# Kernel tuning notes

Measured on AMD Instinct MI355X. Metric: run time of the kernel, lower is better.

## Reference

```python
import jax, jax.numpy as jnp
import numpy as np

NEG_INF = jnp.float32(-(2.0**32) + 1.0)


def squash(z):
    # z: [B, k_max, out_units]
    sq_norm = jnp.sum(jnp.square(z), axis=-1, keepdims=True)
    scale = sq_norm / (1.0 + sq_norm) / jnp.sqrt(sq_norm + 1e-8)
    return scale * z


def setup_inputs() -> dict:
    key = jax.random.key(0)
    k1, k2, k3, k4 = jax.random.split(key, 4)
    B, L, D_IN, D_OUT, K = 1024, 200, 256, 256, 8
    behavior_embeddings = jax.random.normal(k1, (B, L, D_IN), dtype=jnp.float32)
    seq_len = jax.random.randint(k2, (B, 1), 1, L + 1, dtype=jnp.int32)
    routing_logits = jax.random.normal(k3, (1, K, L), dtype=jnp.float32)  # init_std=1.0
    bilinear_mapping_matrix = jax.random.normal(k4, (D_IN, D_OUT), dtype=jnp.float32)
    return {
        "behavior_embeddings": behavior_embeddings,
        "seq_len": seq_len,
        "routing_logits": routing_logits,
        "bilinear_mapping_matrix": bilinear_mapping_matrix,
    }


def reference(behavior_embeddings, seq_len, routing_logits, bilinear_mapping_matrix):
    ITERATION_TIMES = 3
    B, L, _ = behavior_embeddings.shape
    K = routing_logits.shape[1]

    # mask: [B, 1, L] broadcastable to [B, K, L] (same seq_len for every capsule)
    mask = jnp.arange(L)[None, None, :] < seq_len[:, :, None]

    # bilinear map is loop-invariant: [B, L, out_units]
    mapped = jnp.einsum("ble,eo->blo", behavior_embeddings, bilinear_mapping_matrix)

    logits = routing_logits  # [1, K, L]
    interest_capsules = None
    for _ in range(ITERATION_TIMES):
        logits_pad = jnp.where(mask, jnp.broadcast_to(logits, (B, K, L)), NEG_INF)
        weight = jax.nn.softmax(logits_pad, axis=-1)          # [B, K, L]
        Z = jnp.einsum("bkl,blo->bko", weight, mapped)         # [B, K, out]
        interest_capsules = squash(Z)                          # [B, K, out]
        # delta: sum over batch of capsules @ mapped^T -> [1, K, L]
        delta = jnp.einsum("bko,blo->kl", interest_capsules, mapped)[None]
        logits = logits + delta  # emulates assign_add on non-trainable B

    return interest_capsules.reshape(-1, K, interest_capsules.shape[-1])
```

## Files before the change

### kernel.cpp

```cpp
#include <hip/hip_runtime.h>
#include <cstdint>
#include <cstddef>

#define B_    1024
#define L_    200
#define DIN_  256
#define DOUT_ 256
#define K_    8
#define M_    (B_ * L_)

typedef __attribute__((ext_vector_type(8))) short bf16x8;
typedef __attribute__((ext_vector_type(4))) float f32x4;

__device__ __forceinline__ float bf2f(unsigned short u) {
  union { unsigned int i; float f; } w; w.i = ((unsigned int)u) << 16; return w.f;
}
__device__ __forceinline__ unsigned short f2bf(float f) {
  union { float f; unsigned int i; } w; w.f = f;
  unsigned int x = w.i;
  return (unsigned short)((x + 0x7fffu + ((x >> 16) & 1u)) >> 16);
}

__global__ __launch_bounds__(256)
void wt_prep(const float* __restrict__ W, unsigned short* __restrict__ Wh,
             unsigned short* __restrict__ Wm, unsigned short* __restrict__ Wl)
{
  const int k = blockIdx.x;
  const int n = threadIdx.x;
  float x = W[k * DOUT_ + n];
  unsigned short h = f2bf(x);
  float r = x - bf2f(h);
  unsigned short m = f2bf(r);
  float r2 = r - bf2f(m);
  unsigned short l = f2bf(r2);
  const int k0b = k >> 5, quad = (k >> 3) & 3, j = k & 7;
  const int nt = n >> 4, lr = n & 15;
  const size_t idx = ((((size_t)k0b * 16 + nt) * 64) + (quad * 16 + lr)) * 8 + j;
  Wh[idx] = h;
  Wm[idx] = m;
  Wl[idx] = l;
}

__global__ __launch_bounds__(256, 2)
void gemm_mapped(const float* __restrict__ A,
                 const unsigned short* __restrict__ Wh,
                 const unsigned short* __restrict__ Wm,
                 const unsigned short* __restrict__ Wl,
                 float* __restrict__ C)
{
  const int t    = threadIdx.x;
  const int wave = t >> 6;
  const int lane = t & 63;
  const int quad = lane >> 4;
  const int lr   = lane & 15;
  const int m0   = blockIdx.x * 128 + wave * 32;

  f32x4 acc[2][16];
  #pragma unroll
  for (int mt = 0; mt < 2; ++mt)
    #pragma unroll
    for (int nt = 0; nt < 16; ++nt)
      acc[mt][nt] = (f32x4){0.f, 0.f, 0.f, 0.f};

  bf16x8 Bh[4], Bm[4], Bl[4];
  bf16x8 ah[2], am[2], al[2];
  float4 Af[2][2];

#define BLOAD(K0B, NT, S) do { \
    const size_t _off = (((size_t)(K0B) * 16 + (NT)) * 64 + lane) * 8; \
    Bh[S] = *(const bf16x8*)(Wh + _off); \
    Bm[S] = *(const bf16x8*)(Wm + _off); \
    Bl[S] = *(const bf16x8*)(Wl + _off); \
  } while (0)

  const float* ap0 = A + (size_t)(m0 + lr) * DIN_ + quad * 8;
  const float* ap1 = A + (size_t)(m0 + 16 + lr) * DIN_ + quad * 8;

  Af[0][0] = *(const float4*)(ap0);
  Af[0][1] = *(const float4*)(ap0 + 4);
  Af[1][0] = *(const float4*)(ap1);
  Af[1][1] = *(const float4*)(ap1 + 4);
  BLOAD(0, 0, 0); BLOAD(0, 1, 1); BLOAD(0, 2, 2); BLOAD(0, 3, 3);

  for (int k0b = 0; k0b < 8; ++k0b) {
    #pragma unroll
    for (int mt = 0; mt < 2; ++mt) {
      float xs[8] = {Af[mt][0].x, Af[mt][0].y, Af[mt][0].z, Af[mt][0].w,
                     Af[mt][1].x, Af[mt][1].y, Af[mt][1].z, Af[mt][1].w};
      #pragma unroll
      for (int j = 0; j < 8; ++j) {
        unsigned short h = f2bf(xs[j]);
        float r = xs[j] - bf2f(h);
        unsigned short mm = f2bf(r);
        float r2 = r - bf2f(mm);
        unsigned short ll = f2bf(r2);
        ah[mt][j] = (short)h; am[mt][j] = (short)mm; al[mt][j] = (short)ll;
      }
    }
    if (k0b < 7) {
      const int ko = (k0b + 1) * 32;
      Af[0][0] = *(const float4*)(ap0 + ko);
      Af[0][1] = *(const float4*)(ap0 + ko + 4);
      Af[1][0] = *(const float4*)(ap1 + ko);
      Af[1][1] = *(const float4*)(ap1 + ko + 4);
    }

#define GROUP(NT, S) do { \
    f32x4 c0 = acc[0][NT], c1 = acc[1][NT]; \
    c0 = __builtin_amdgcn_mfma_f32_16x16x32_bf16(ah[0], Bh[S], c0, 0, 0, 0); \
    c1 = __builtin_amdgcn_mfma_f32_16x16x32_bf16(ah[1], Bh[S], c1, 0, 0, 0); \
    c0 = __builtin_amdgcn_mfma_f32_16x16x32_bf16(ah[0], Bm[S], c0, 0, 0, 0); \
    c1 = __builtin_amdgcn_mfma_f32_16x16x32_bf16(ah[1], Bm[S], c1, 0, 0, 0); \
    c0 = __builtin_amdgcn_mfma_f32_16x16x32_bf16(am[0], Bh[S], c0, 0, 0, 0); \
    c1 = __builtin_amdgcn_mfma_f32_16x16x32_bf16(am[1], Bh[S], c1, 0, 0, 0); \
    c0 = __builtin_amdgcn_mfma_f32_16x16x32_bf16(ah[0], Bl[S], c0, 0, 0, 0); \
    c1 = __builtin_amdgcn_mfma_f32_16x16x32_bf16(ah[1], Bl[S], c1, 0, 0, 0); \
    c0 = __builtin_amdgcn_mfma_f32_16x16x32_bf16(am[0], Bm[S], c0, 0, 0, 0); \
    c1 = __builtin_amdgcn_mfma_f32_16x16x32_bf16(am[1], Bm[S], c1, 0, 0, 0); \
    c0 = __builtin_amdgcn_mfma_f32_16x16x32_bf16(al[0], Bh[S], c0, 0, 0, 0); \
    c1 = __builtin_amdgcn_mfma_f32_16x16x32_bf16(al[1], Bh[S], c1, 0, 0, 0); \
    acc[0][NT] = c0; acc[1][NT] = c1; \
  } while (0)

    GROUP(0, 0);  BLOAD(k0b, 4, 0);
    GROUP(1, 1);  BLOAD(k0b, 5, 1);
    GROUP(2, 2);  BLOAD(k0b, 6, 2);
    GROUP(3, 3);  BLOAD(k0b, 7, 3);
    GROUP(4, 0);  BLOAD(k0b, 8, 0);
    GROUP(5, 1);  BLOAD(k0b, 9, 1);
    GROUP(6, 2);  BLOAD(k0b, 10, 2);
    GROUP(7, 3);  BLOAD(k0b, 11, 3);
    GROUP(8, 0);  BLOAD(k0b, 12, 0);
    GROUP(9, 1);  BLOAD(k0b, 13, 1);
    GROUP(10, 2); BLOAD(k0b, 14, 2);
    GROUP(11, 3); BLOAD(k0b, 15, 3);
    GROUP(12, 0);
    GROUP(13, 1);
    GROUP(14, 2);
    GROUP(15, 3);
    if (k0b < 7) {
      BLOAD(k0b + 1, 0, 0); BLOAD(k0b + 1, 1, 1);
      BLOAD(k0b + 1, 2, 2); BLOAD(k0b + 1, 3, 3);
    }
#undef GROUP
  }
#undef BLOAD

  #pragma unroll
  for (int mt = 0; mt < 2; ++mt)
    #pragma unroll
    for (int nt = 0; nt < 16; ++nt)
      #pragma unroll
      for (int r = 0; r < 4; ++r) {
        int row = m0 + mt * 16 + quad * 4 + r;
        C[(size_t)row * DOUT_ + nt * 16 + lr] = acc[mt][nt][r];
      }
}

__global__ __launch_bounds__(256)
void z_kernel(const float* __restrict__ mapped, const float* __restrict__ logits,
              const int* __restrict__ seq_len, float* __restrict__ caps)
{
  const int t    = threadIdx.x;
  const int lane = t & 63;
  const int wave = t >> 6;
  const int b    = blockIdx.x * 4 + wave;
  const int len  = seq_len[b];
  __shared__ float w[4][K_][204];

  #pragma unroll
  for (int k = 0; k < K_; ++k) {
    float v[4];
    float mx = -3.4028235e38f;
    #pragma unroll
    for (int i = 0; i < 4; ++i) {
      int l = lane + 64 * i;
      v[i] = (l < len) ? logits[k * L_ + l] : -3.4028235e38f;
      mx = fmaxf(mx, v[i]);
    }
    #pragma unroll
    for (int s = 1; s < 64; s <<= 1) mx = fmaxf(mx, __shfl_xor(mx, s, 64));
    float e[4]; float sum = 0.f;
    #pragma unroll
    for (int i = 0; i < 4; ++i) {
      int l = lane + 64 * i;
      e[i] = (l < len) ? __expf(v[i] - mx) : 0.f;
      sum += e[i];
    }
    #pragma unroll
    for (int s = 1; s < 64; s <<= 1) sum += __shfl_xor(sum, s, 64);
    float inv = 1.f / sum;
    #pragma unroll
    for (int i = 0; i < 4; ++i) {
      int l = lane + 64 * i;
      if (l < 204) w[wave][k][l] = e[i] * inv;
    }
  }

  f32x4 acc[K_];
  #pragma unroll
  for (int k = 0; k < K_; ++k) acc[k] = (f32x4){0.f, 0.f, 0.f, 0.f};
  const float* mp = mapped + (size_t)b * L_ * DOUT_ + lane * 4;
  const int lceil = (len + 3) & ~3;
  for (int l = 0; l < lceil; l += 4) {
    float4 m0 = *(const float4*)(mp + (size_t)(l + 0) * DOUT_);
    float4 m1 = *(const float4*)(mp + (size_t)(l + 1) * DOUT_);
    float4 m2 = *(const float4*)(mp + (size_t)(l + 2) * DOUT_);
    float4 m3 = *(const float4*)(mp + (size_t)(l + 3) * DOUT_);
    #pragma unroll
    for (int k = 0; k < K_; ++k) {
      float4 wv = *(const float4*)&w[wave][k][l];
      f32x4 c = acc[k];
      c.x += wv.x * m0.x + wv.y * m1.x + wv.z * m2.x + wv.w * m3.x;
      c.y += wv.x * m0.y + wv.y * m1.y + wv.z * m2.y + wv.w * m3.y;
      c.z += wv.x * m0.z + wv.y * m1.z + wv.z * m2.z + wv.w * m3.z;
      c.w += wv.x * m0.w + wv.y * m1.w + wv.z * m2.w + wv.w * m3.w;
      acc[k] = c;
    }
  }

  #pragma unroll
  for (int k = 0; k < K_; ++k) {
    float sq = acc[k].x * acc[k].x + acc[k].y * acc[k].y
             + acc[k].z * acc[k].z + acc[k].w * acc[k].w;
    #pragma unroll
    for (int s = 1; s < 64; s <<= 1) sq += __shfl_xor(sq, s, 64);
    float scale = sq / ((1.f + sq) * sqrtf(sq + 1e-8f));
    float4 o;
    o.x = scale * acc[k].x; o.y = scale * acc[k].y;
    o.z = scale * acc[k].z; o.w = scale * acc[k].w;
    *(float4*)&caps[((size_t)b * K_ + k) * DOUT_ + lane * 4] = o;
  }
}

__global__ __launch_bounds__(256)
void delta_kernel(const float* __restrict__ mapped, const float* __restrict__ caps,
                  float* __restrict__ partials)
{
  const int t    = threadIdx.x;
  const int lane = t & 63;
  const int wave = t >> 6;
  const int wid  = blockIdx.x * 4 + wave;
  const int lc   = wid % 25;
  const int bc   = wid / 25;
  const int l0   = lc * 8;
  const int o4   = lane * 4;

  const float* cb = caps   + (size_t)(bc * 16) * (K_ * DOUT_) + o4;
  const float* mb = mapped + ((size_t)(bc * 16) * L_ + l0) * DOUT_ + o4;

  float acc[K_][8];
  #pragma unroll
  for (int k = 0; k < K_; ++k)
    #pragma unroll
    for (int ll = 0; ll < 8; ++ll) acc[k][ll] = 0.f;

  float4 cA[K_], mA[8], cB[K_], mB[8];

#define LOADC(DST, BI) do { \
    const float* _p = cb + (size_t)(BI) * (K_ * DOUT_); \
    _Pragma("unroll") \
    for (int _k = 0; _k < K_; ++_k) DST[_k] = *(const float4*)(_p + _k * DOUT_); \
  } while (0)
#define LOADM(DST, BI) do { \
    const float* _p = mb + (size_t)(BI) * (L_ * DOUT_); \
    _Pragma("unroll") \
    for (int _l = 0; _l < 8; ++_l) DST[_l] = *(const float4*)(_p + _l * DOUT_); \
  } while (0)
#define COMPUTE(CC, MM) do { \
    _Pragma("unroll") \
    for (int _k = 0; _k < K_; ++_k) \
      _Pragma("unroll") \
      for (int _l = 0; _l < 8; ++_l) \
        acc[_k][_l] += CC[_k].x * MM[_l].x + CC[_k].y * MM[_l].y \
                     + CC[_k].z * MM[_l].z + CC[_k].w * MM[_l].w; \
  } while (0)

  LOADC(cA, 0); LOADM(mA, 0);
  for (int i = 0; i < 8; ++i) {
    LOADC(cB, 2 * i + 1); LOADM(mB, 2 * i + 1);
    COMPUTE(cA, mA);
    if (i < 7) { LOADC(cA, 2 * i + 2); LOADM(mA, 2 * i + 2); }
    COMPUTE(cB, mB);
  }
#undef LOADC
#undef LOADM
#undef COMPUTE

  float out = 0.f;
  #pragma unroll
  for (int k = 0; k < K_; ++k)
    #pragma unroll
    for (int ll = 0; ll < 8; ++ll) {
      float v = acc[k][ll];
      v += __shfl_xor(v, 1, 64);
      v += __shfl_xor(v, 2, 64);
      v += __shfl_xor(v, 4, 64);
      v += __shfl_xor(v, 8, 64);
      v += __shfl_xor(v, 16, 64);
      v += __shfl_xor(v, 32, 64);
      if (lane == k * 8 + ll) out = v;
    }
  partials[((size_t)bc * K_ + (lane >> 3)) * L_ + l0 + (lane & 7)] = out;
}

__global__ __launch_bounds__(256)
void init_logits(const float* __restrict__ rlog, float* __restrict__ logits)
{
  int i = blockIdx.x * 256 + threadIdx.x;
  if (i < K_ * L_) logits[i] = rlog[i];
}

__global__ __launch_bounds__(256)
void reduce_kernel(const float* __restrict__ partials, float* __restrict__ logits)
{
  int i = blockIdx.x * 256 + threadIdx.x;
  if (i < K_ * L_) {
    float s = 0.f;
    #pragma unroll 4
    for (int bc = 0; bc < 64; ++bc) s += partials[bc * (K_ * L_) + i];
    logits[i] += s;
  }
}

extern "C" void kernel_launch(void* const* d_in, const int* in_sizes, int n_in,
                              void* d_out, int out_size, void* d_ws, size_t ws_size,
                              hipStream_t stream)
{
  const float* behav = (const float*)d_in[0];
  const int*   slen  = (const int*)d_in[1];
  const float* rlog  = (const float*)d_in[2];
  const float* W     = (const float*)d_in[3];
  float* caps = (float*)d_out;

  char* ws = (char*)d_ws;
  float* logitsW  = (float*)ws;
  float* partials = (float*)(ws + 8192);
  unsigned short* Wh = (unsigned short*)(ws + 458752);
  unsigned short* Wm = (unsigned short*)(ws + 589824);
  unsigned short* Wl = (unsigned short*)(ws + 720896);
  float* mapped   = (float*)(ws + (1 << 20));

  init_logits<<<dim3(7), 256, 0, stream>>>(rlog, logitsW);
  wt_prep<<<dim3(256), 256, 0, stream>>>(W, Wh, Wm, Wl);
  gemm_mapped<<<dim3(1600), 256, 0, stream>>>(behav, Wh, Wm, Wl, mapped);
  for (int it = 0; it < 3; ++it) {
    z_kernel<<<dim3(B_ / 4), 256, 0, stream>>>(mapped, logitsW, slen, caps);
    if (it < 2) {
      delta_kernel<<<dim3(400), 256, 0, stream>>>(mapped, caps, partials);
      reduce_kernel<<<dim3(7), 256, 0, stream>>>(partials, logitsW);
    }
  }
}
```

Baseline: 637.5 us.

## Fuse routing z and delta into one kernel with fixed-point atomic accumulation

Merges the capsule computation and the delta reduction into one per-batch kernel. Logit updates are accumulated via int64 fixed-point atomics instead of a partials buffer plus reduce kernel, and the z phase is restructured to one block per batch with waves splitting the sequence. This removes the separate delta and reduce launches and the caps round trip, at the cost of many contended global atomics and per-row wave shuffle reductions.

```diff
diff --git a/kernel.cpp b/kernel.cpp
--- a/kernel.cpp
+++ b/kernel.cpp
@@ -157,26 +157,45 @@
       }
 }
 
-__global__ __launch_bounds__(256)
-void z_kernel(const float* __restrict__ mapped, const float* __restrict__ logits,
-              const int* __restrict__ seq_len, float* __restrict__ caps)
+#define DSCALE     67108864.0f
+#define DSCALE_INV 1.4901161193847656e-8f
+
+template<bool DO_DELTA>
+__global__ __launch_bounds__(256, 4)
+void zdelta_kernel(const float* __restrict__ mapped,
+                   const float* __restrict__ rlog,
+                   const long long* __restrict__ accA,
+                   const long long* __restrict__ accB,
+                   const int* __restrict__ seq_len,
+                   long long* __restrict__ accOut,
+                   float* __restrict__ caps)
 {
   const int t    = threadIdx.x;
   const int lane = t & 63;
   const int wave = t >> 6;
-  const int b    = blockIdx.x * 4 + wave;
+  const int b    = blockIdx.x;
   const int len  = seq_len[b];
-  __shared__ float w[4][K_][204];
-
-  #pragma unroll
-  for (int k = 0; k < K_; ++k) {
+
+  __shared__ float wsmT[200][8];
+  __shared__ float zred[2][8][256];
+  __shared__ float capsL[8][256];
+  __shared__ float sqred[4][8];
+
+  #pragma unroll
+  for (int kk = 0; kk < 2; ++kk) {
+    const int k = wave * 2 + kk;
     float v[4];
     float mx = -3.4028235e38f;
     #pragma unroll
     for (int i = 0; i < 4; ++i) {
       int l = lane + 64 * i;
-      v[i] = (l < len) ? logits[k * L_ + l] : -3.4028235e38f;
-      mx = fmaxf(mx, v[i]);
+      float lv = -3.4028235e38f;
+      if (l < len) {
+        long long a = accA[(k * L_ + l) * 8] + accB[(k * L_ + l) * 8];
+        lv = rlog[k * L_ + l] + (float)a * DSCALE_INV;
+      }
+      v[i] = lv;
+      mx = fmaxf(mx, lv);
     }
     #pragma unroll
     for (int s = 1; s < 64; s <<= 1) mx = fmaxf(mx, __shfl_xor(mx, s, 64));
@@ -193,134 +212,91 @@
     #pragma unroll
     for (int i = 0; i < 4; ++i) {
       int l = lane + 64 * i;
-      if (l < 204) w[wave][k][l] = e[i] * inv;
-    }
-  }
-
-  f32x4 acc[K_];
-  #pragma unroll
-  for (int k = 0; k < K_; ++k) acc[k] = (f32x4){0.f, 0.f, 0.f, 0.f};
-  const float* mp = mapped + (size_t)b * L_ * DOUT_ + lane * 4;
-  const int lceil = (len + 3) & ~3;
-  for (int l = 0; l < lceil; l += 4) {
-    float4 m0 = *(const float4*)(mp + (size_t)(l + 0) * DOUT_);
-    float4 m1 = *(const float4*)(mp + (size_t)(l + 1) * DOUT_);
-    float4 m2 = *(const float4*)(mp + (size_t)(l + 2) * DOUT_);
-    float4 m3 = *(const float4*)(mp + (size_t)(l + 3) * DOUT_);
+      if (l < L_) wsmT[l][k] = e[i] * inv;
+    }
+  }
+  __syncthreads();
+
+  f32x4 zacc[K_];
+  #pragma unroll
+  for (int k = 0; k < K_; ++k) zacc[k] = (f32x4){0.f, 0.f, 0.f, 0.f};
+
+  const float* mp = mapped + (size_t)b * (L_ * DOUT_) + lane * 4;
+  for (int l = wave; l < len; l += 4) {
+    f32x4 m = *(const f32x4*)(mp + (size_t)l * DOUT_);
+    float4 w0 = *(const float4*)&wsmT[l][0];
+    float4 w1 = *(const float4*)&wsmT[l][4];
+    zacc[0] += w0.x * m; zacc[1] += w0.y * m;
+    zacc[2] += w0.z * m; zacc[3] += w0.w * m;
+    zacc[4] += w1.x * m; zacc[5] += w1.y * m;
+    zacc[6] += w1.z * m; zacc[7] += w1.w * m;
+  }
+
+  if (wave >= 2) {
+    #pragma unroll
+    for (int k = 0; k < K_; ++k)
+      *(f32x4*)&zred[wave - 2][k][lane * 4] = zacc[k];
+  }
+  __syncthreads();
+  if (wave < 2) {
     #pragma unroll
     for (int k = 0; k < K_; ++k) {
-      float4 wv = *(const float4*)&w[wave][k][l];
-      f32x4 c = acc[k];
-      c.x += wv.x * m0.x + wv.y * m1.x + wv.z * m2.x + wv.w * m3.x;
-      c.y += wv.x * m0.y + wv.y * m1.y + wv.z * m2.y + wv.w * m3.y;
-      c.z += wv.x * m0.z + wv.y * m1.z + wv.z * m2.z + wv.w * m3.z;
-      c.w += wv.x * m0.w + wv.y * m1.w + wv.z * m2.w + wv.w * m3.w;
-      acc[k] = c;
-    }
-  }
+      f32x4 r = *(const f32x4*)&zred[wave][k][lane * 4];
+      r += zacc[k];
+      *(f32x4*)&zred[wave][k][lane * 4] = r;
+    }
+  }
+  __syncthreads();
+
+  float z[K_];
+  #pragma unroll
+  for (int k = 0; k < K_; ++k) z[k] = zred[0][k][t] + zred[1][k][t];
 
   #pragma unroll
   for (int k = 0; k < K_; ++k) {
-    float sq = acc[k].x * acc[k].x + acc[k].y * acc[k].y
-             + acc[k].z * acc[k].z + acc[k].w * acc[k].w;
-    #pragma unroll
-    for (int s = 1; s < 64; s <<= 1) sq += __shfl_xor(sq, s, 64);
+    float s2 = z[k] * z[k];
+    #pragma unroll
+    for (int s = 1; s < 64; s <<= 1) s2 += __shfl_xor(s2, s, 64);
+    if (lane == 0) sqred[wave][k] = s2;
+  }
+  __syncthreads();
+  #pragma unroll
+  for (int k = 0; k < K_; ++k) {
+    float sq = sqred[0][k] + sqred[1][k] + sqred[2][k] + sqred[3][k];
     float scale = sq / ((1.f + sq) * sqrtf(sq + 1e-8f));
-    float4 o;
-    o.x = scale * acc[k].x; o.y = scale * acc[k].y;
-    o.z = scale * acc[k].z; o.w = scale * acc[k].w;
-    *(float4*)&caps[((size_t)b * K_ + k) * DOUT_ + lane * 4] = o;
+    float cv = scale * z[k];
+    if (DO_DELTA) capsL[k][t] = cv;
+    else caps[((size_t)b * K_ + k) * DOUT_ + t] = cv;
+  }
+
+  if constexpr (DO_DELTA) {
+    __syncthreads();
+    f32x4 cr[K_];
+    #pragma unroll
+    for (int k = 0; k < K_; ++k) cr[k] = *(const f32x4*)&capsL[k][lane * 4];
+
+    for (int l = wave; l < L_; l += 4) {
+      f32x4 m = *(const f32x4*)(mp + (size_t)l * DOUT_);
+      #pragma unroll
+      for (int k = 0; k < K_; ++k) {
+        float p = cr[k].x * m.x + cr[k].y * m.y + cr[k].z * m.z + cr[k].w * m.w;
+        #pragma unroll
+        for (int s = 1; s < 64; s <<= 1) p += __shfl_xor(p, s, 64);
+        if (lane == 0) {
+          long long q = llrintf(p * DSCALE);
+          atomicAdd((unsigned long long*)&accOut[(k * L_ + l) * 8],
+                    (unsigned long long)q);
+        }
+      }
+    }
   }
 }
 
 __global__ __launch_bounds__(256)
-void delta_kernel(const float* __restrict__ mapped, const float* __restrict__ caps,
-                  float* __restrict__ partials)
-{
-  const int t    = threadIdx.x;
-  const int lane = t & 63;
-  const int wave = t >> 6;
-  const int wid  = blockIdx.x * 4 + wave;
-  const int lc   = wid % 25;
-  const int bc   = wid / 25;
-  const int l0   = lc * 8;
-  const int o4   = lane * 4;
-
-  const float* cb = caps   + (size_t)(bc * 16) * (K_ * DOUT_) + o4;
-  const float* mb = mapped + ((size_t)(bc * 16) * L_ + l0) * DOUT_ + o4;
-
-  float acc[K_][8];
-  #pragma unroll
-  for (int k = 0; k < K_; ++k)
-    #pragma unroll
-    for (int ll = 0; ll < 8; ++ll) acc[k][ll] = 0.f;
-
-  float4 cA[K_], mA[8], cB[K_], mB[8];
-
-#define LOADC(DST, BI) do { \
-    const float* _p = cb + (size_t)(BI) * (K_ * DOUT_); \
-    _Pragma("unroll") \
-    for (int _k = 0; _k < K_; ++_k) DST[_k] = *(const float4*)(_p + _k * DOUT_); \
-  } while (0)
-#define LOADM(DST, BI) do { \
-    const float* _p = mb + (size_t)(BI) * (L_ * DOUT_); \
-    _Pragma("unroll") \
-    for (int _l = 0; _l < 8; ++_l) DST[_l] = *(const float4*)(_p + _l * DOUT_); \
-  } while (0)
-#define COMPUTE(CC, MM) do { \
-    _Pragma("unroll") \
-    for (int _k = 0; _k < K_; ++_k) \
-      _Pragma("unroll") \
-      for (int _l = 0; _l < 8; ++_l) \
-        acc[_k][_l] += CC[_k].x * MM[_l].x + CC[_k].y * MM[_l].y \
-                     + CC[_k].z * MM[_l].z + CC[_k].w * MM[_l].w; \
-  } while (0)
-
-  LOADC(cA, 0); LOADM(mA, 0);
-  for (int i = 0; i < 8; ++i) {
-    LOADC(cB, 2 * i + 1); LOADM(mB, 2 * i + 1);
-    COMPUTE(cA, mA);
-    if (i < 7) { LOADC(cA, 2 * i + 2); LOADM(mA, 2 * i + 2); }
-    COMPUTE(cB, mB);
-  }
-#undef LOADC
-#undef LOADM
-#undef COMPUTE
-
-  float out = 0.f;
-  #pragma unroll
-  for (int k = 0; k < K_; ++k)
-    #pragma unroll
-    for (int ll = 0; ll < 8; ++ll) {
-      float v = acc[k][ll];
-      v += __shfl_xor(v, 1, 64);
-      v += __shfl_xor(v, 2, 64);
-      v += __shfl_xor(v, 4, 64);
-      v += __shfl_xor(v, 8, 64);
-      v += __shfl_xor(v, 16, 64);
-      v += __shfl_xor(v, 32, 64);
-      if (lane == k * 8 + ll) out = v;
-    }
-  partials[((size_t)bc * K_ + (lane >> 3)) * L_ + l0 + (lane & 7)] = out;
-}
-
-__global__ __launch_bounds__(256)
-void init_logits(const float* __restrict__ rlog, float* __restrict__ logits)
+void init_acc(long long* __restrict__ a)
 {
   int i = blockIdx.x * 256 + threadIdx.x;
-  if (i < K_ * L_) logits[i] = rlog[i];
-}
-
-__global__ __launch_bounds__(256)
-void reduce_kernel(const float* __restrict__ partials, float* __restrict__ logits)
-{
-  int i = blockIdx.x * 256 + threadIdx.x;
-  if (i < K_ * L_) {
-    float s = 0.f;
-    #pragma unroll 4
-    for (int bc = 0; bc < 64; ++bc) s += partials[bc * (K_ * L_) + i];
-    logits[i] += s;
-  }
+  a[i] = 0;
 }
 
 extern "C" void kernel_launch(void* const* d_in, const int* in_sizes, int n_in,
@@ -334,21 +310,19 @@
   float* caps = (float*)d_out;
 
   char* ws = (char*)d_ws;
-  float* logitsW  = (float*)ws;
-  float* partials = (float*)(ws + 8192);
-  unsigned short* Wh = (unsigned short*)(ws + 458752);
-  unsigned short* Wm = (unsigned short*)(ws + 589824);
-  unsigned short* Wl = (unsigned short*)(ws + 720896);
+  long long* z0   = (long long*)ws;
+  long long* acc0 = (long long*)(ws + 102400);
+  long long* acc1 = (long long*)(ws + 204800);
+  unsigned short* Wh = (unsigned short*)(ws + 327680);
+  unsigned short* Wm = (unsigned short*)(ws + 458752);
+  unsigned short* Wl = (unsigned short*)(ws + 589824);
   float* mapped   = (float*)(ws + (1 << 20));
 
-  init_logits<<<dim3(7), 256, 0, stream>>>(rlog, logitsW);
+  init_acc<<<dim3(150), 256, 0, stream>>>((long long*)ws);
   wt_prep<<<dim3(256), 256, 0, stream>>>(W, Wh, Wm, Wl);
   gemm_mapped<<<dim3(1600), 256, 0, stream>>>(behav, Wh, Wm, Wl, mapped);
-  for (int it = 0; it < 3; ++it) {
-    z_kernel<<<dim3(B_ / 4), 256, 0, stream>>>(mapped, logitsW, slen, caps);
-    if (it < 2) {
-      delta_kernel<<<dim3(400), 256, 0, stream>>>(mapped, caps, partials);
-      reduce_kernel<<<dim3(7), 256, 0, stream>>>(partials, logitsW);
-    }
-  }
-}
+
+  zdelta_kernel<true ><<<dim3(B_), 256, 0, stream>>>(mapped, rlog, z0,   z0,   slen, acc0, nullptr);
+  zdelta_kernel<true ><<<dim3(B_), 256, 0, stream>>>(mapped, rlog, acc0, z0,   slen, acc1, nullptr);
+  zdelta_kernel<false><<<dim3(B_), 256, 0, stream>>>(mapped, rlog, acc0, acc1, slen, nullptr, caps);
+}
```

Result: slower. 844.4 us (+32.5%).
